# Kernel tuning notes

Hardware: AMD Instinct MI355X
Metric: run time of the kernel (lower is better)

The kernel has to match this reference:

```python
import jax, jax.numpy as jnp
import numpy as np
import math

B, C, A, W, H = 8, 128, 16, 64, 64


def setup_inputs() -> dict:
    key = jax.random.key(0)
    ks = jax.random.split(key, 7)
    s_in = 1.0 / math.sqrt(C)
    return {
        "x": jax.random.normal(ks[0], (B, C, W, H), dtype=jnp.float32),
        "Wq": jax.random.normal(ks[1], (A, C), dtype=jnp.float32) * s_in,
        "bq": jnp.zeros((A,), dtype=jnp.float32),
        "Wk": jax.random.normal(ks[2], (A, C), dtype=jnp.float32) * s_in,
        "bk": jnp.zeros((A,), dtype=jnp.float32),
        "Wv": jax.random.normal(ks[3], (C, C), dtype=jnp.float32) * s_in,
        "bv": jnp.zeros((C,), dtype=jnp.float32),
    }


def reference(x, Wq, bq, Wk, bk, Wv, bv):
    # 1x1 convs == per-pixel linear projections
    q = jnp.einsum('ac,bcwh->bawh', Wq, x) + bq[None, :, None, None]  # [B,A,W,H]
    k = jnp.einsum('ac,bcwh->bawh', Wk, x) + bk[None, :, None, None]  # [B,A,W,H]
    v = jnp.einsum('vc,bcwh->bvwh', Wv, x) + bv[None, :, None, None]  # [B,C,W,H]

    scale = 1.0 / math.sqrt(q.shape[1])
    # full spatial attention: [B, W, H, W, H]
    attn = jnp.einsum('bawh,baWH->bwhWH', q, k)
    b, w, h, _, _ = attn.shape
    attn = jax.nn.softmax(attn.reshape(b, w, h, -1) * scale, axis=-1)
    attn = attn.reshape(b, w, h, w, h)
    out = jnp.einsum('bwhWH,bvWH->bvwh', attn, v)  # [B,C,W,H]
    return out
```

## Files before the change

### kernel.cpp

```cpp
#include <hip/hip_runtime.h>
#include <math.h>

#define BB 8
#define CC 128
#define NN 4096

typedef _Float16 f16;
typedef _Float16 f16x4v __attribute__((ext_vector_type(4)));
typedef _Float16 f16x8 __attribute__((ext_vector_type(8)));
typedef float f32x4v __attribute__((ext_vector_type(4)));
typedef float f32x16 __attribute__((ext_vector_type(16)));

#if __has_builtin(__builtin_amdgcn_exp2f)
#define EXP2(x) __builtin_amdgcn_exp2f(x)
#else
#define EXP2(x) __expf((x)*0.69314718056f)
#endif

#define QSCALE 0.360673760222f
#define SHIFT  5.770780163555f

#define WF_BYTES 65536

__global__ __launch_bounds__(256)
void prep_kernel(const float* __restrict__ Wq, const float* __restrict__ bq,
                 const float* __restrict__ Wk, const float* __restrict__ bk,
                 const float* __restrict__ Wv, const float* __restrict__ bv,
                 f16* __restrict__ Wf, float* __restrict__ biasS)
{
    const int tg = blockIdx.x*256 + threadIdx.x;
    if (tg < 2560) {
        const int mt = tg >> 9, ks = (tg >> 6) & 7, l = tg & 63;
        const int n32 = l & 31, h = l >> 5;
        const int r = mt*32 + n32;
        f16x8 v8;
        #pragma unroll
        for (int i = 0; i < 8; i++) {
            int c = ks*16 + 8*h + i;
            float wv_;
            if (r < 16)      wv_ = QSCALE * Wq[r*CC + c];
            else if (r < 32) wv_ = Wk[(r-16)*CC + c];
            else             wv_ = Wv[(r-32)*CC + c];
            v8[i] = (f16)wv_;
        }
        *(f16x8*)&Wf[(size_t)tg*8] = v8;
    }
    if (blockIdx.x == 0 && threadIdx.x < 160) {
        int r = threadIdx.x;
        biasS[r] = r < 16 ? QSCALE*bq[r] : (r < 32 ? bk[r-16] : bv[r-32]);
    }
}

__global__ __launch_bounds__(256)
void proj_kernel(const float* __restrict__ x, const f16* __restrict__ Wf,
                 const float* __restrict__ biasS,
                 f16* __restrict__ Qt, f16* __restrict__ Kt, f16* __restrict__ Vf)
{
    __shared__ __align__(16) f16 Vl[CC*140];

    const int tid  = threadIdx.x;
    const int lane = tid & 63;
    const int wv   = tid >> 6;
    const int b    = blockIdx.x & 7;
    const int pt   = blockIdx.x >> 3;
    const int n32  = lane & 31;
    const int half = lane >> 5;
    const int p    = pt*128 + wv*32 + n32;

    const float* xp = x + (size_t)b*CC*NN + p;
    f16x8 xf[8];
    #pragma unroll
    for (int ks = 0; ks < 8; ks++) {
        float xv[8];
        #pragma unroll
        for (int i = 0; i < 8; i++)
            xv[i] = __builtin_nontemporal_load(&xp[(size_t)(ks*16 + 8*half + i)*NN]);
        #pragma unroll
        for (int i = 0; i < 8; i++) xf[ks][i] = (f16)xv[i];
    }

    f32x16 acc[5];
    #pragma unroll
    for (int mt = 0; mt < 5; mt++) acc[mt] = (f32x16)0.0f;
    #pragma unroll
    for (int ks = 0; ks < 8; ks++) {
        #pragma unroll
        for (int mt = 0; mt < 5; mt++) {
            f16x8 wfr = *(const f16x8*)&Wf[((size_t)(mt*8 + ks)*64 + lane)*8];
            acc[mt] = __builtin_amdgcn_mfma_f32_32x32x16_f16(wfr, xf[ks], acc[mt], 0, 0, 0);
        }
    }

    #pragma unroll
    for (int mt = 0; mt < 5; mt++) {
        #pragma unroll
        for (int q = 0; q < 4; q++) {
            float4 b4 = *(const float4*)&biasS[mt*32 + q*8 + 4*half];
            acc[mt][q*4+0] += b4.x; acc[mt][q*4+1] += b4.y;
            acc[mt][q*4+2] += b4.z; acc[mt][q*4+3] += b4.w;
        }
    }

    {
        size_t qkoff = ((size_t)b*NN + p)*16;
        f16x4v s0, s1, s2, s3;
        #pragma unroll
        for (int i = 0; i < 4; i++) {
            s0[i] = (f16)acc[0][i];    s1[i] = (f16)acc[0][4+i];
            s2[i] = (f16)acc[0][8+i];  s3[i] = (f16)acc[0][12+i];
        }
        *(f16x4v*)&Qt[qkoff + 4*half]     = s0;
        *(f16x4v*)&Qt[qkoff + 8 + 4*half] = s1;
        *(f16x4v*)&Kt[qkoff + 4*half]     = s2;
        *(f16x4v*)&Kt[qkoff + 8 + 4*half] = s3;
    }

    #pragma unroll
    for (int mt = 1; mt < 5; mt++) {
        #pragma unroll
        for (int g = 0; g < 16; g++) {
            int c = (mt-1)*32 + (g & 3) + 8*(g >> 2) + 4*half;
            Vl[c*140 + wv*32 + n32] = (f16)acc[mt][g];
        }
    }
    __syncthreads();

    #pragma unroll
    for (int pass = 0; pass < 8; pass++) {
        int item = pass*256 + tid;
        int l    = item & 63;
        int f    = (item >> 6) & 15;
        int ktl  = item >> 10;
        int c16  = f >> 2, ct = f & 3;
        int li   = l & 31, h2 = l >> 5;
        const f16* src = &Vl[(ct*32 + li)*140 + ktl*64 + c16*16 + 4*h2];
        f16x4v lo = *(const f16x4v*)&src[0];
        f16x4v hi = *(const f16x4v*)&src[8];
        f16x8 v8;
        #pragma unroll
        for (int i = 0; i < 4; i++) { v8[i] = lo[i]; v8[4+i] = hi[i]; }
        int ktg = pt*2 + ktl;
        *(f16x8*)&Vf[((((size_t)b*64 + ktg)*16 + c16*4 + ct)*64 + l)*8] = v8;
    }
}

__global__ __launch_bounds__(256, 2)
void attn_kernel(const f16* __restrict__ Qt, const f16* __restrict__ Kt,
                 const f16* __restrict__ Vf, float* __restrict__ out)
{
    __shared__ __align__(16) unsigned char lds_raw[27776];

    const int tid  = threadIdx.x;
    const int lane = tid & 63;
    const int wv   = tid >> 6;
    const int b    = blockIdx.x & 7;
    const int qt   = blockIdx.x >> 3;
    const int q0   = qt*32;
    const int n32  = lane & 31;
    const int half = lane >> 5;

    const f16* vb = Vf + (size_t)b*64*16*512;
    const f16* kb = Kt + (size_t)b*NN*16;
    const f16x8 qf = *(const f16x8*)&Qt[((size_t)b*NN + q0 + n32)*16 + half*8];

    f32x16 of[4];
    #pragma unroll
    for (int ct = 0; ct < 4; ct++) of[ct] = (f32x16)0.0f;
    float ps[4] = {0.f, 0.f, 0.f, 0.f};

    f16x8 kf0 = *(const f16x8*)&kb[((size_t)wv*64 + n32)*16 + half*8];
    f16x8 kf1 = *(const f16x8*)&kb[((size_t)wv*64 + 32 + n32)*16 + half*8];
    f16x8 vpf[16];
    {
        const f16* vt = vb + (size_t)wv*8192;
        #pragma unroll
        for (int i = 0; i < 16; i++)
            vpf[i] = *(const f16x8*)&vt[((size_t)i*64 + lane)*8];
    }

    for (int kt = wv; kt < NN/64; kt += 4) {
        const int ktn = (kt + 4 < NN/64) ? kt + 4 : kt;
        f16x8 kf0n = *(const f16x8*)&kb[((size_t)ktn*64 + n32)*16 + half*8];
        f16x8 kf1n = *(const f16x8*)&kb[((size_t)ktn*64 + 32 + n32)*16 + half*8];

        f32x16 St0 = __builtin_amdgcn_mfma_f32_32x32x16_f16(kf0, qf, (f32x16)(-SHIFT), 0, 0, 0);
        f32x16 St1 = __builtin_amdgcn_mfma_f32_32x32x16_f16(kf1, qf, (f32x16)(-SHIFT), 0, 0, 0);

        f16x8 pf[4];
        #pragma unroll
        for (int g = 0; g < 16; g++) {
            float e0 = EXP2(St0[g]); ps[g & 3] += e0; pf[(g >> 3)][g & 7]     = (f16)e0;
            float e1 = EXP2(St1[g]); ps[g & 3] += e1; pf[2 + (g >> 3)][g & 7] = (f16)e1;
        }

        const f16* vtn = vb + (size_t)ktn*8192;
        #pragma unroll
        for (int kc = 0; kc < 4; kc++) {
            #pragma unroll
            for (int ct = 0; ct < 4; ct++) {
                const int i = kc*4 + ct;
                f16x8 vc = vpf[i];
                vpf[i] = *(const f16x8*)&vtn[((size_t)i*64 + lane)*8];
                of[ct] = __builtin_amdgcn_mfma_f32_32x32x16_f16(pf[kc], vc, of[ct], 0, 0, 0);
            }
        }
        kf0 = kf0n; kf1 = kf1n;
    }

    float ls = (ps[0] + ps[1]) + (ps[2] + ps[3]);
    ls += __shfl_xor(ls, 32);

    __syncthreads();
    if (wv != 0) {
        unsigned char* base = lds_raw + (size_t)(wv-1)*9216 + (size_t)lane*144;
        #pragma unroll
        for (int ct = 0; ct < 4; ct++) {
            #pragma unroll
            for (int h = 0; h < 2; h++) {
                f16x8 t;
                #pragma unroll
                for (int jj = 0; jj < 8; jj++) t[jj] = (f16)of[ct][h*8+jj];
                *(f16x8*)(base + ct*32 + h*16) = t;
            }
        }
        *(float*)(base + 128) = ls;
    }
    __syncthreads();
    if (wv == 0) {
        #pragma unroll
        for (int s2 = 0; s2 < 3; s2++) {
            unsigned char* base = lds_raw + (size_t)s2*9216 + (size_t)lane*144;
            #pragma unroll
            for (int ct = 0; ct < 4; ct++) {
                #pragma unroll
                for (int h = 0; h < 2; h++) {
                    f16x8 t = *(const f16x8*)(base + ct*32 + h*16);
                    #pragma unroll
                    for (int jj = 0; jj < 8; jj++) of[ct][h*8+jj] += (float)t[jj];
                }
            }
            ls += *(const float*)(base + 128);
        }
        float* ls_inv = (float*)(lds_raw + 27648);
        if (lane < 32) ls_inv[lane] = 1.f / ls;
        float invq[16];
        #pragma unroll
        for (int g = 0; g < 16; g++)
            invq[g] = ls_inv[(g & 3) + 8*(g >> 2) + 4*half];
        float* Tb = (float*)lds_raw;
        #pragma unroll
        for (int ct = 0; ct < 4; ct++) {
            #pragma unroll
            for (int g = 0; g < 16; g++) {
                int row = (g & 3) + 8*(g >> 2) + 4*half;
                Tb[(ct*32 + n32)*36 + row] = of[ct][g] * invq[g];
            }
        }
    }
    __syncthreads();
    {
        const float* Tb = (const float*)lds_raw;
        #pragma unroll
        for (int it = 0; it < 4; it++) {
            int idx = it*256 + tid;
            int c = idx >> 3, qq = idx & 7;
            f32x4v v = *(const f32x4v*)&Tb[c*36 + qq*4];
            __builtin_nontemporal_store(v,
                (f32x4v*)&out[((size_t)b*CC + c)*NN + q0 + qq*4]);
        }
    }
}

extern "C" void kernel_launch(void* const* d_in, const int* in_sizes, int n_in,
                              void* d_out, int out_size, void* d_ws, size_t ws_size,
                              hipStream_t stream) {
    const float* x  = (const float*)d_in[0];
    const float* Wq = (const float*)d_in[1];
    const float* bq = (const float*)d_in[2];
    const float* Wk = (const float*)d_in[3];
    const float* bk = (const float*)d_in[4];
    const float* Wv = (const float*)d_in[5];
    const float* bv = (const float*)d_in[6];
    float* out = (float*)d_out;

    f16* Qw = (f16*)d_ws;
    f16* Kw = Qw + (size_t)BB*NN*16;
    f16* Vw = Kw + (size_t)BB*NN*16;
    unsigned char* tail = (unsigned char*)d_out + (size_t)out_size*4 - WF_BYTES;
    f16*   Wf    = (f16*)tail;
    float* biasS = (float*)(tail + 49152);

    hipLaunchKernelGGL(prep_kernel, dim3(10), dim3(256), 0, stream,
                       Wq, bq, Wk, bk, Wv, bv, Wf, biasS);
    hipLaunchKernelGGL(proj_kernel, dim3(256), dim3(256), 0, stream,
                       x, Wf, biasS, Qw, Kw, Vw);
    hipLaunchKernelGGL(attn_kernel, dim3(1024), dim3(256), 0, stream,
                       Qw, Kw, Vw, out);
}
```

Before: 136.7 us.

## Widen attention tile to 128 queries with LDS-exchanged probabilities across waves

Measured after the change: 133.8 us. 2.1% less time.

```diff
diff --git a/kernel.cpp b/kernel.cpp
--- a/kernel.cpp
+++ b/kernel.cpp
@@ -144,130 +144,158 @@
     }
 }
 
-__global__ __launch_bounds__(256, 2)
+__global__ __launch_bounds__(512, 1)
 void attn_kernel(const f16* __restrict__ Qt, const f16* __restrict__ Kt,
                  const f16* __restrict__ Vf, float* __restrict__ out)
 {
-    __shared__ __align__(16) unsigned char lds_raw[27776];
+    __shared__ __align__(16) unsigned char lds_raw[65536];
 
     const int tid  = threadIdx.x;
     const int lane = tid & 63;
-    const int wv   = tid >> 6;
+    const int w    = tid >> 6;
+    const int ct   = w & 3;
+    const int kh   = w >> 2;
     const int b    = blockIdx.x & 7;
     const int qt   = blockIdx.x >> 3;
-    const int q0   = qt*32;
+    const int q0   = qt*128;
     const int n32  = lane & 31;
     const int half = lane >> 5;
 
     const f16* vb = Vf + (size_t)b*64*16*512;
     const f16* kb = Kt + (size_t)b*NN*16;
-    const f16x8 qf = *(const f16x8*)&Qt[((size_t)b*NN + q0 + n32)*16 + half*8];
-
-    f32x16 of[4];
-    #pragma unroll
-    for (int ct = 0; ct < 4; ct++) of[ct] = (f32x16)0.0f;
+    const f16x8 qf = *(const f16x8*)&Qt[((size_t)b*NN + q0 + ct*32 + n32)*16 + half*8];
+
+    f32x16 of0 = (f32x16)0.0f, of1 = (f32x16)0.0f;
+    f32x16 of2 = (f32x16)0.0f, of3 = (f32x16)0.0f;
     float ps[4] = {0.f, 0.f, 0.f, 0.f};
 
-    f16x8 kf0 = *(const f16x8*)&kb[((size_t)wv*64 + n32)*16 + half*8];
-    f16x8 kf1 = *(const f16x8*)&kb[((size_t)wv*64 + 32 + n32)*16 + half*8];
-    f16x8 vpf[16];
+    f16* Pex = (f16*)lds_raw;
+
+    f16x8 kfA0 = *(const f16x8*)&kb[((size_t)(kh)*64 + n32)*16 + half*8];
+    f16x8 kfA1 = *(const f16x8*)&kb[((size_t)(kh)*64 + 32 + n32)*16 + half*8];
+    f16x8 kfB0 = *(const f16x8*)&kb[((size_t)(kh+2)*64 + n32)*16 + half*8];
+    f16x8 kfB1 = *(const f16x8*)&kb[((size_t)(kh+2)*64 + 32 + n32)*16 + half*8];
+    f16x8 vpfA[4], vpfB[4];
     {
-        const f16* vt = vb + (size_t)wv*8192;
-        #pragma unroll
-        for (int i = 0; i < 16; i++)
-            vpf[i] = *(const f16x8*)&vt[((size_t)i*64 + lane)*8];
-    }
-
-    for (int kt = wv; kt < NN/64; kt += 4) {
-        const int ktn = (kt + 4 < NN/64) ? kt + 4 : kt;
-        f16x8 kf0n = *(const f16x8*)&kb[((size_t)ktn*64 + n32)*16 + half*8];
-        f16x8 kf1n = *(const f16x8*)&kb[((size_t)ktn*64 + 32 + n32)*16 + half*8];
-
-        f32x16 St0 = __builtin_amdgcn_mfma_f32_32x32x16_f16(kf0, qf, (f32x16)(-SHIFT), 0, 0, 0);
-        f32x16 St1 = __builtin_amdgcn_mfma_f32_32x32x16_f16(kf1, qf, (f32x16)(-SHIFT), 0, 0, 0);
-
-        f16x8 pf[4];
-        #pragma unroll
-        for (int g = 0; g < 16; g++) {
-            float e0 = EXP2(St0[g]); ps[g & 3] += e0; pf[(g >> 3)][g & 7]     = (f16)e0;
-            float e1 = EXP2(St1[g]); ps[g & 3] += e1; pf[2 + (g >> 3)][g & 7] = (f16)e1;
-        }
-
-        const f16* vtn = vb + (size_t)ktn*8192;
+        const f16* vtA = vb + (size_t)(kh)*8192;
+        const f16* vtB = vb + (size_t)(kh+2)*8192;
         #pragma unroll
         for (int kc = 0; kc < 4; kc++) {
-            #pragma unroll
-            for (int ct = 0; ct < 4; ct++) {
-                const int i = kc*4 + ct;
-                f16x8 vc = vpf[i];
-                vpf[i] = *(const f16x8*)&vtn[((size_t)i*64 + lane)*8];
-                of[ct] = __builtin_amdgcn_mfma_f32_32x32x16_f16(pf[kc], vc, of[ct], 0, 0, 0);
-            }
-        }
-        kf0 = kf0n; kf1 = kf1n;
-    }
+            vpfA[kc] = *(const f16x8*)&vtA[((size_t)(kc*4 + ct)*64 + lane)*8];
+            vpfB[kc] = *(const f16x8*)&vtB[((size_t)(kc*4 + ct)*64 + lane)*8];
+        }
+    }
+
+#define STEP(T, KF0, KF1, VPF, PB)                                                    \
+    {                                                                                 \
+        f32x16 St0 = __builtin_amdgcn_mfma_f32_32x32x16_f16(KF0, qf, (f32x16)(-SHIFT), 0, 0, 0); \
+        f32x16 St1 = __builtin_amdgcn_mfma_f32_32x32x16_f16(KF1, qf, (f32x16)(-SHIFT), 0, 0, 0); \
+        int tl = (T) + 4; if (tl > 63) tl = (T);                                      \
+        KF0 = *(const f16x8*)&kb[((size_t)tl*64 + n32)*16 + half*8];                  \
+        KF1 = *(const f16x8*)&kb[((size_t)tl*64 + 32 + n32)*16 + half*8];             \
+        f16x8 po[4];                                                                  \
+        _Pragma("unroll")                                                             \
+        for (int g = 0; g < 16; g++) {                                                \
+            float e0 = EXP2(St0[g]); ps[g & 3] += e0; po[(g >> 3)][g & 7]     = (f16)e0; \
+            float e1 = EXP2(St1[g]); ps[g & 3] += e1; po[2 + (g >> 3)][g & 7] = (f16)e1; \
+        }                                                                             \
+        {                                                                             \
+            f16* wr = &Pex[(((size_t)((PB)*2 + kh)*16 + ct*4)*64 + lane)*8];          \
+            _Pragma("unroll")                                                         \
+            for (int kc = 0; kc < 4; kc++) *(f16x8*)&wr[kc*512] = po[kc];             \
+        }                                                                             \
+        asm volatile("s_waitcnt lgkmcnt(0)\n\ts_barrier" ::: "memory");               \
+        const f16* vtn = vb + (size_t)tl*8192;                                        \
+        _Pragma("unroll")                                                             \
+        for (int kc = 0; kc < 4; kc++) {                                              \
+            f16x8 vc = VPF[kc];                                                       \
+            VPF[kc] = *(const f16x8*)&vtn[((size_t)(kc*4 + ct)*64 + lane)*8];         \
+            const f16* rdb = &Pex[(((size_t)((PB)*2 + kh)*16 + kc)*64 + lane)*8];     \
+            f16x8 p0 = *(const f16x8*)&rdb[0*4*512];                                  \
+            f16x8 p1 = *(const f16x8*)&rdb[1*4*512];                                  \
+            f16x8 p2 = *(const f16x8*)&rdb[2*4*512];                                  \
+            f16x8 p3 = *(const f16x8*)&rdb[3*4*512];                                  \
+            of0 = __builtin_amdgcn_mfma_f32_32x32x16_f16(p0, vc, of0, 0, 0, 0);       \
+            of1 = __builtin_amdgcn_mfma_f32_32x32x16_f16(p1, vc, of1, 0, 0, 0);       \
+            of2 = __builtin_amdgcn_mfma_f32_32x32x16_f16(p2, vc, of2, 0, 0, 0);       \
+            of3 = __builtin_amdgcn_mfma_f32_32x32x16_f16(p3, vc, of3, 0, 0, 0);       \
+        }                                                                             \
+    }
+
+    for (int i = 0; i < 16; ++i) {
+        const int t = 4*i + kh;
+        STEP(t,     kfA0, kfA1, vpfA, 0)
+        STEP(t + 2, kfB0, kfB1, vpfB, 1)
+    }
+#undef STEP
 
     float ls = (ps[0] + ps[1]) + (ps[2] + ps[3]);
     ls += __shfl_xor(ls, 32);
 
     __syncthreads();
-    if (wv != 0) {
-        unsigned char* base = lds_raw + (size_t)(wv-1)*9216 + (size_t)lane*144;
-        #pragma unroll
-        for (int ct = 0; ct < 4; ct++) {
+    float* lsb = (float*)(lds_raw + 36864);
+    if (lane < 32) lsb[w*32 + n32] = ls;
+    if (kh == 1) {
+        unsigned char* base = lds_raw + (size_t)ct*9216 + (size_t)lane*144;
+        #pragma unroll
+        for (int s = 0; s < 4; s++) {
+            const f32x16& o = s == 0 ? of0 : (s == 1 ? of1 : (s == 2 ? of2 : of3));
             #pragma unroll
             for (int h = 0; h < 2; h++) {
-                f16x8 t;
+                f16x8 tv;
                 #pragma unroll
-                for (int jj = 0; jj < 8; jj++) t[jj] = (f16)of[ct][h*8+jj];
-                *(f16x8*)(base + ct*32 + h*16) = t;
+                for (int jj = 0; jj < 8; jj++) tv[jj] = (f16)o[h*8 + jj];
+                *(f16x8*)(base + s*32 + h*16) = tv;
             }
         }
-        *(float*)(base + 128) = ls;
     }
     __syncthreads();
-    if (wv == 0) {
-        #pragma unroll
-        for (int s2 = 0; s2 < 3; s2++) {
-            unsigned char* base = lds_raw + (size_t)s2*9216 + (size_t)lane*144;
+    float* ls_inv = (float*)(lds_raw + 37888);
+    if (kh == 0) {
+        unsigned char* base = lds_raw + (size_t)ct*9216 + (size_t)lane*144;
+        #pragma unroll
+        for (int s = 0; s < 4; s++) {
+            f32x16& o = s == 0 ? of0 : (s == 1 ? of1 : (s == 2 ? of2 : of3));
             #pragma unroll
-            for (int ct = 0; ct < 4; ct++) {
+            for (int h = 0; h < 2; h++) {
+                f16x8 tv = *(const f16x8*)(base + s*32 + h*16);
                 #pragma unroll
-                for (int h = 0; h < 2; h++) {
-                    f16x8 t = *(const f16x8*)(base + ct*32 + h*16);
+                for (int jj = 0; jj < 8; jj++) o[h*8 + jj] += (float)tv[jj];
+            }
+        }
+        if (lane < 32)
+            ls_inv[ct*32 + n32] = 1.f / (lsb[w*32 + n32] + lsb[(w+4)*32 + n32]);
+    }
+    __syncthreads();
+
+    float* Tb = (float*)lds_raw;
+    #pragma unroll
+    for (int pass = 0; pass < 2; pass++) {
+        if (kh == 0) {
+            #pragma unroll
+            for (int sl = 0; sl < 2; sl++) {
+                const int s = pass*2 + sl;
+                const f32x16& o = s == 0 ? of0 : (s == 1 ? of1 : (s == 2 ? of2 : of3));
+                #pragma unroll
+                for (int j = 0; j < 4; j++) {
+                    f32x4v iv = *(const f32x4v*)&ls_inv[s*32 + 8*j + 4*half];
+                    f32x4v ov;
                     #pragma unroll
-                    for (int jj = 0; jj < 8; jj++) of[ct][h*8+jj] += (float)t[jj];
+                    for (int e = 0; e < 4; e++) ov[e] = o[4*j + e] * iv[e];
+                    *(f32x4v*)&Tb[(size_t)(ct*32 + n32)*68 + sl*32 + 8*j + 4*half] = ov;
                 }
             }
-            ls += *(const float*)(base + 128);
-        }
-        float* ls_inv = (float*)(lds_raw + 27648);
-        if (lane < 32) ls_inv[lane] = 1.f / ls;
-        float invq[16];
-        #pragma unroll
-        for (int g = 0; g < 16; g++)
-            invq[g] = ls_inv[(g & 3) + 8*(g >> 2) + 4*half];
-        float* Tb = (float*)lds_raw;
-        #pragma unroll
-        for (int ct = 0; ct < 4; ct++) {
-            #pragma unroll
-            for (int g = 0; g < 16; g++) {
-                int row = (g & 3) + 8*(g >> 2) + 4*half;
-                Tb[(ct*32 + n32)*36 + row] = of[ct][g] * invq[g];
-            }
-        }
-    }
-    __syncthreads();
-    {
-        const float* Tb = (const float*)lds_raw;
+        }
+        __syncthreads();
         #pragma unroll
         for (int it = 0; it < 4; it++) {
-            int idx = it*256 + tid;
-            int c = idx >> 3, qq = idx & 7;
-            f32x4v v = *(const f32x4v*)&Tb[c*36 + qq*4];
+            int idx = it*512 + tid;
+            int c = idx >> 4, qg = idx & 15;
+            f32x4v v = *(const f32x4v*)&Tb[(size_t)c*68 + qg*4];
             __builtin_nontemporal_store(v,
-                (f32x4v*)&out[((size_t)b*CC + c)*NN + q0 + qq*4]);
-        }
+                (f32x4v*)&out[((size_t)b*CC + c)*NN + q0 + pass*64 + qg*4]);
+        }
+        if (pass == 0) __syncthreads();
     }
 }
 
@@ -294,6 +322,6 @@
                        Wq, bq, Wk, bk, Wv, bv, Wf, biasS);
     hipLaunchKernelGGL(proj_kernel, dim3(256), dim3(256), 0, stream,
                        x, Wf, biasS, Qw, Kw, Vw);
-    hipLaunchKernelGGL(attn_kernel, dim3(1024), dim3(256), 0, stream,
+    hipLaunchKernelGGL(attn_kernel, dim3(256), dim3(512), 0, stream,
                        Qw, Kw, Vw, out);
 }
```
